# Performance work log

Hardware: AMD Instinct MI355X
Metric: run time of the kernel (lower is better)

Reference implementation:

```python
import jax, jax.numpy as jnp
import numpy as np

N = 50000      # nodes
E = 800000     # edges (avg degree 16)
F_IN = 256
F_OUT = 256


def setup_inputs() -> dict:
    key = jax.random.key(0)
    ks = jax.random.split(key, 8)
    feature = jax.random.normal(ks[0], (N, F_IN), dtype=jnp.float32)
    e_w = jax.random.uniform(ks[1], (E, 1), dtype=jnp.float32)
    snorm_n = jnp.ones((N, 1), dtype=jnp.float32)
    snorm_e = jnp.ones((E, 1), dtype=jnp.float32)
    src = jax.random.randint(ks[2], (E,), 0, N, dtype=jnp.int32)
    dst = jax.random.randint(ks[3], (E,), 0, N, dtype=jnp.int32)
    scale = 1.0 / np.sqrt(F_IN)
    W_self = jax.random.normal(ks[4], (F_IN, F_OUT), dtype=jnp.float32) * scale
    W = jax.random.normal(ks[5], (F_IN, F_OUT), dtype=jnp.float32) * scale
    b = jax.random.normal(ks[6], (F_OUT,), dtype=jnp.float32) * scale
    return {"feature": feature, "e_w": e_w, "snorm_n": snorm_n,
            "snorm_e": snorm_e, "W_self": W_self, "W": W, "b": b,
            "src": src, "dst": dst}


def reference(feature, e_w, snorm_n, snorm_e, W_self, W, b, src, dst):
    n = feature.shape[0]
    ones_e = jnp.ones_like(src, dtype=feature.dtype)
    # self transform
    h_s = feature @ W_self                                   # [N, F_OUT]
    # source-side degree normalization: deg_out^{-1/2}
    out_deg = jnp.maximum(jax.ops.segment_sum(ones_e, src, num_segments=n), 1.0)
    feat = feature * (out_deg ** -0.5)[:, None]              # [N, F_IN]
    # message = h[src] * e_w, aggregated by sum into dst (u_mul_e + sum reduce)
    msgs = feat[src] * e_w                                   # [E, F_IN]
    agg = jax.ops.segment_sum(msgs, dst, num_segments=n)     # [N, F_IN]
    # neighbor transform + destination-side degree normalization
    h = agg @ W + b                                          # [N, F_OUT]
    in_deg = jnp.maximum(jax.ops.segment_sum(ones_e, dst, num_segments=n), 1.0)
    h = h * (in_deg ** -0.5)[:, None]
    return h_s + h, e_w
```

## Files before the change

kernel.cpp:

```cpp
#include <hip/hip_runtime.h>
#include <hip/hip_bf16.h>

#define N_NODES 50000
#define N_EDGES 800000

#define ROW_TILES    391
#define K1_BLOCKS    2352
#define WCONV_BLOCKS 512
#define SCAN_BLOCKS  196
#define EDGE_BLOCKS  782

typedef __bf16 bf16x8_t __attribute__((ext_vector_type(8)));
typedef float  f32x4_t  __attribute__((ext_vector_type(4)));
typedef unsigned short u16x8 __attribute__((ext_vector_type(8)));
typedef unsigned int   u32x4 __attribute__((ext_vector_type(4)));

__device__ __forceinline__ unsigned short f2bf(float x) {
  __hip_bfloat16 h = __float2bfloat16(x);
  return __builtin_bit_cast(unsigned short, h);
}
__device__ __forceinline__ float bf2f(unsigned short u) {
  unsigned int v = ((unsigned int)u) << 16;
  return __builtin_bit_cast(float, v);
}
__device__ __forceinline__ unsigned int pk2(float lo, float hi) {
  return ((unsigned int)f2bf(hi) << 16) | (unsigned int)f2bf(lo);
}
__device__ __forceinline__ bf16x8_t cvt8(float4 lo, float4 hi) {
  u32x4 u;
  u.x = pk2(lo.x, lo.y); u.y = pk2(lo.z, lo.w);
  u.z = pk2(hi.x, hi.y); u.w = pk2(hi.z, hi.w);
  return __builtin_bit_cast(bf16x8_t, u);
}

__global__ __launch_bounds__(256) void wconv_kernel(
    const float* __restrict__ Wself, const float* __restrict__ W,
    unsigned short* __restrict__ Bt)
{
  int idx = blockIdx.x * 256 + threadIdx.x;
  int n = idx >> 8, k = idx & 255;
  float v = (n < 256) ? Wself[k * 256 + n] : W[k * 256 + (n - 256)];
  Bt[idx] = f2bf(v);
}

__global__ __launch_bounds__(256, 4) void gemm_edge_kernel(
    const float* __restrict__ feature,
    const unsigned short* __restrict__ Bt,
    const float* __restrict__ e_w, const int* __restrict__ src, const int* __restrict__ dst,
    int* __restrict__ cnt_in, int* __restrict__ cnt_out,
    unsigned char* __restrict__ rank8, float* __restrict__ out1,
    unsigned short* __restrict__ hs16,
    unsigned char* __restrict__ y8)
{
  const int b   = blockIdx.x;
  const int tid = threadIdx.x;
  const int w   = b / 48;
  const int o   = (b % 48) >> 3;
  const int r   = b & 7;

  if (o == 2 || o == 5) {
    const int h = w * 16 + r + ((o == 5) ? 8 : 0);
    if (h >= EDGE_BLOCKS) return;
    const int e0 = h * 1024 + tid;
#pragma unroll
    for (int k = 0; k < 4; ++k) {
      int e = e0 + k * 256;
      if (e < N_EDGES) {
        int s = src[e], d = dst[e];
        out1[e] = e_w[e];
        atomicAdd(&cnt_out[s], 1);
        rank8[e] = (unsigned char)atomicAdd(&cnt_in[d], 1);
      }
    }
    return;
  }

  const int q = o - (o > 2 ? 1 : 0);
  const int t = w * 8 + r;
  if (t >= ROW_TILES) return;

  const int m0   = t * 128;
  const int bn0  = q * 128;
  const int lane = tid & 63;
  const int wave = tid >> 6;
  const int wm   = (wave & 1) * 64;
  const int wn   = (wave >> 1) * 64;
  const int fr   = lane & 15;
  const int fkc  = lane >> 4;

  const float* ap[4];
  const unsigned short* bp[4];
#pragma unroll
  for (int i = 0; i < 4; ++i) {
    int row = m0 + wm + i * 16 + fr;
    row = (row < N_NODES) ? row : 0;
    ap[i] = feature + (size_t)row * 256 + fkc * 8;
  }
#pragma unroll
  for (int j = 0; j < 4; ++j)
    bp[j] = Bt + (size_t)(bn0 + wn + j * 16 + fr) * 256 + fkc * 8;

  f32x4_t acc[4][4] = {};

  for (int s = 0; s < 8; ++s) {
    const int k0 = s * 32;
    bf16x8_t av[4], bv[4];
#pragma unroll
    for (int i = 0; i < 4; ++i) {
      float4 lo = *(const float4*)(ap[i] + k0);
      float4 hi = *(const float4*)(ap[i] + k0 + 4);
      av[i] = cvt8(lo, hi);
    }
#pragma unroll
    for (int j = 0; j < 4; ++j)
      bv[j] = *(const bf16x8_t*)(bp[j] + k0);
#pragma unroll
    for (int i = 0; i < 4; ++i)
#pragma unroll
      for (int j = 0; j < 4; ++j)
        acc[i][j] = __builtin_amdgcn_mfma_f32_16x16x32_bf16(av[i], bv[j], acc[i][j], 0, 0, 0);
  }

  if (q < 2) {
    const int cbase = q * 128 + wn + (lane & 15);
#pragma unroll
    for (int i = 0; i < 4; ++i) {
      int rowb = m0 + wm + i * 16 + (lane >> 4) * 4;
#pragma unroll
      for (int j = 0; j < 4; ++j) {
        int col = cbase + j * 16;
#pragma unroll
        for (int rr = 0; rr < 4; ++rr) {
          int row = rowb + rr;
          if (row < N_NODES)
            hs16[(size_t)row * 256 + col] = f2bf(acc[i][j][rr]);
        }
      }
    }
  } else {
    const int cbase = (q - 2) * 128 + wn + (lane & 15);
#pragma unroll
    for (int i = 0; i < 4; ++i) {
      int rowb = m0 + wm + i * 16 + (lane >> 4) * 4;
#pragma unroll
      for (int j = 0; j < 4; ++j) {
        int col = cbase + j * 16;
#pragma unroll
        for (int rr = 0; rr < 4; ++rr) {
          int row = rowb + rr;
          if (row < N_NODES) {
            float ys = acc[i][j][rr];
            unsigned int pk = (unsigned int)__builtin_amdgcn_cvt_pk_fp8_f32(ys, ys, 0, false);
            y8[(size_t)row * 256 + col] = (unsigned char)(pk & 0xffu);
          }
        }
      }
    }
  }
}

__global__ __launch_bounds__(256) void scan1_kernel(
    const int* __restrict__ cnt, int* __restrict__ sums)
{
  int idx = blockIdx.x * 256 + threadIdx.x;
  int v = (idx < N_NODES) ? cnt[idx] : 0;
#pragma unroll
  for (int d = 32; d; d >>= 1) v += __shfl_down(v, d);
  __shared__ int sm[4];
  if ((threadIdx.x & 63) == 0) sm[threadIdx.x >> 6] = v;
  __syncthreads();
  if (threadIdx.x == 0) sums[blockIdx.x] = sm[0] + sm[1] + sm[2] + sm[3];
}

__global__ __launch_bounds__(256) void scan2_kernel(int* __restrict__ sums)
{
  const int t = threadIdx.x;
  int v = (t < SCAN_BLOCKS) ? sums[t] : 0;
  __shared__ int sm[256];
  sm[t] = v;
  __syncthreads();
  for (int d = 1; d < 256; d <<= 1) {
    int u = (t >= d) ? sm[t - d] : 0;
    __syncthreads();
    sm[t] += u;
    __syncthreads();
  }
  if (t < SCAN_BLOCKS) sums[t] = sm[t] - v;
}

__global__ __launch_bounds__(256) void scan3_kernel(
    const int* __restrict__ cnt, const int* __restrict__ sums, int* __restrict__ off)
{
  const int t = threadIdx.x;
  int idx = blockIdx.x * 256 + t;
  int v = (idx < N_NODES) ? cnt[idx] : 0;
  __shared__ int sm[256];
  sm[t] = v;
  __syncthreads();
  for (int d = 1; d < 256; d <<= 1) {
    int u = (t >= d) ? sm[t - d] : 0;
    __syncthreads();
    sm[t] += u;
    __syncthreads();
  }
  if (idx <= N_NODES) off[idx] = sm[t] - v + sums[blockIdx.x];
}

__global__ __launch_bounds__(256) void scatter_kernel(
    const float* __restrict__ e_w, const int* __restrict__ src, const int* __restrict__ dst,
    const unsigned char* __restrict__ rank8, const int* __restrict__ off,
    unsigned int* __restrict__ csr)
{
  const int e0 = blockIdx.x * 1024 + threadIdx.x;
#pragma unroll
  for (int k = 0; k < 4; ++k) {
    int e = e0 + k * 256;
    if (e < N_EDGES) {
      int d = dst[e];
      int r = rank8[e];
      float w = e_w[e];
      int s = src[e];
      csr[off[d] + r] = ((unsigned int)f2bf(w) << 16) | (unsigned int)s;
    }
  }
}

__global__ __launch_bounds__(256) void agg_kernel(
    const unsigned char* __restrict__ y8, const unsigned int* __restrict__ csr,
    const int* __restrict__ off, const int* __restrict__ cnt_out,
    const unsigned short* __restrict__ hs16,
    const float* __restrict__ bias, float* __restrict__ out0)
{
  const int hw   = threadIdx.x >> 5;
  const int lane = threadIdx.x & 31;
  const int node = blockIdx.x * 8 + hw;
  if (node >= N_NODES) return;
  const int base = off[node];
  const int deg  = off[node + 1] - base;

  float a0 = 0.f, a1 = 0.f, a2 = 0.f, a3 = 0.f;
  float a4 = 0.f, a5 = 0.f, a6 = 0.f, a7 = 0.f;

  for (int bb = 0; bb < deg; bb += 32) {
    int idx = bb + lane;
    unsigned int ent = (idx < deg) ? csr[base + idx] : 0u;
    int   sl = (int)(ent & 0xffffu);
    float wl = bf2f((unsigned short)(ent >> 16));
    int co = cnt_out[sl]; if (co < 1) co = 1;
    wl *= rsqrtf((float)co);

#pragma unroll
    for (int t0 = 0; t0 < 32; t0 += 16) {
      if (bb + t0 >= deg) break;
#pragma unroll
      for (int t = 0; t < 16; ++t) {
        int eb = t0 + t;
        int   s = __shfl(sl, eb, 32);
        float w = __shfl(wl, eb, 32);
        uint2 u = *(const uint2*)(y8 + (size_t)s * 256 + lane * 8);
        a0 += w * __builtin_amdgcn_cvt_f32_fp8(u.x, 0);
        a1 += w * __builtin_amdgcn_cvt_f32_fp8(u.x, 1);
        a2 += w * __builtin_amdgcn_cvt_f32_fp8(u.x, 2);
        a3 += w * __builtin_amdgcn_cvt_f32_fp8(u.x, 3);
        a4 += w * __builtin_amdgcn_cvt_f32_fp8(u.y, 0);
        a5 += w * __builtin_amdgcn_cvt_f32_fp8(u.y, 1);
        a6 += w * __builtin_amdgcn_cvt_f32_fp8(u.y, 2);
        a7 += w * __builtin_amdgcn_cvt_f32_fp8(u.y, 3);
      }
    }
  }

  int dn = deg < 1 ? 1 : deg;
  float inv = rsqrtf((float)dn);
  size_t offo = (size_t)node * 256 + lane * 8;
  u16x8 hv = *(const u16x8*)(hs16 + offo);
  float4 b0 = *(const float4*)(bias + lane * 8);
  float4 b1 = *(const float4*)(bias + lane * 8 + 4);
  float4 o0, o1;
  o0.x = bf2f(hv[0]) + (a0 + b0.x) * inv;
  o0.y = bf2f(hv[1]) + (a1 + b0.y) * inv;
  o0.z = bf2f(hv[2]) + (a2 + b0.z) * inv;
  o0.w = bf2f(hv[3]) + (a3 + b0.w) * inv;
  o1.x = bf2f(hv[4]) + (a4 + b1.x) * inv;
  o1.y = bf2f(hv[5]) + (a5 + b1.y) * inv;
  o1.z = bf2f(hv[6]) + (a6 + b1.z) * inv;
  o1.w = bf2f(hv[7]) + (a7 + b1.w) * inv;
  *(float4*)(out0 + offo)     = o0;
  *(float4*)(out0 + offo + 4) = o1;
}

extern "C" void kernel_launch(void* const* d_in, const int* in_sizes, int n_in,
                              void* d_out, int out_size, void* d_ws, size_t ws_size,
                              hipStream_t stream) {
  const float* feature = (const float*)d_in[0];
  const float* e_w     = (const float*)d_in[1];
  const float* W_self  = (const float*)d_in[4];
  const float* W       = (const float*)d_in[5];
  const float* bias    = (const float*)d_in[6];
  const int*   src     = (const int*)d_in[7];
  const int*   dst     = (const int*)d_in[8];

  float* out0 = (float*)d_out;
  float* out1 = out0 + (size_t)N_NODES * 256;

  char* ws = (char*)d_ws;
  int*            cnt_in  = (int*)(ws + 0);
  int*            cnt_out = (int*)(ws + 262144);
  int*            off     = (int*)(ws + 524288);
  unsigned char*  rank8   = (unsigned char*)(ws + 786432);
  int*            sums    = (int*)(ws + 1638400);
  unsigned int*   csr     = (unsigned int*)(ws + 1835008);
  unsigned short* Bt      = (unsigned short*)(ws + 5242880);
  unsigned char*  y8      = (unsigned char*)(ws + 5767168);
  unsigned short* hs16    = (unsigned short*)(ws + 18567168);

  hipMemsetAsync(ws, 0, 524288, stream);

  wconv_kernel<<<WCONV_BLOCKS, 256, 0, stream>>>(W_self, W, Bt);
  gemm_edge_kernel<<<K1_BLOCKS, 256, 0, stream>>>(
      feature, Bt, e_w, src, dst, cnt_in, cnt_out, rank8, out1, hs16, y8);
  scan1_kernel<<<SCAN_BLOCKS, 256, 0, stream>>>(cnt_in, sums);
  scan2_kernel<<<1, 256, 0, stream>>>(sums);
  scan3_kernel<<<SCAN_BLOCKS, 256, 0, stream>>>(cnt_in, sums, off);
  scatter_kernel<<<EDGE_BLOCKS, 256, 0, stream>>>(e_w, src, dst, rank8, off, csr);
  agg_kernel<<<(N_NODES + 7) / 8, 256, 0, stream>>>(y8, csr, off, cnt_out, hs16, bias, out0);
}
```

Baseline: 304.8 us.

## Stage B tile in swizzled LDS, preload A, fold out-degree norm into CSR

Result: faster. 290.0 us (-4.9%).

```diff
diff --git a/kernel.cpp b/kernel.cpp
--- a/kernel.cpp
+++ b/kernel.cpp
@@ -43,7 +43,7 @@
   Bt[idx] = f2bf(v);
 }
 
-__global__ __launch_bounds__(256, 4) void gemm_edge_kernel(
+__global__ __launch_bounds__(256, 2) void gemm_edge_kernel(
     const float* __restrict__ feature,
     const unsigned short* __restrict__ Bt,
     const float* __restrict__ e_w, const int* __restrict__ src, const int* __restrict__ dst,
@@ -75,6 +75,8 @@
     return;
   }
 
+  __shared__ __align__(16) unsigned short Bs[128 * 256];
+
   const int q = o - (o > 2 ? 1 : 0);
   const int t = w * 8 + r;
   if (t >= ROW_TILES) return;
@@ -88,37 +90,51 @@
   const int fr   = lane & 15;
   const int fkc  = lane >> 4;
 
+#pragma unroll
+  for (int m = 0; m < 16; ++m) {
+    int L  = m * 256 + tid;
+    int rr = L >> 5, cs = L & 31;
+    int cg = cs ^ (rr & 7);
+    const unsigned short* gb = Bt + (size_t)(bn0 + rr) * 256 + cg * 8;
+    __builtin_amdgcn_global_load_lds((const __attribute__((address_space(1))) void*)gb,
+                                     (__attribute__((address_space(3))) void*)&Bs[(size_t)L * 8],
+                                     16, 0, 0);
+  }
+
   const float* ap[4];
-  const unsigned short* bp[4];
 #pragma unroll
   for (int i = 0; i < 4; ++i) {
     int row = m0 + wm + i * 16 + fr;
     row = (row < N_NODES) ? row : 0;
     ap[i] = feature + (size_t)row * 256 + fkc * 8;
   }
-#pragma unroll
-  for (int j = 0; j < 4; ++j)
-    bp[j] = Bt + (size_t)(bn0 + wn + j * 16 + fr) * 256 + fkc * 8;
+  bf16x8_t Areg[8][4];
+#pragma unroll
+  for (int s = 0; s < 8; ++s)
+#pragma unroll
+    for (int i = 0; i < 4; ++i) {
+      float4 lo = *(const float4*)(ap[i] + s * 32);
+      float4 hi = *(const float4*)(ap[i] + s * 32 + 4);
+      Areg[s][i] = cvt8(lo, hi);
+    }
+
+  __syncthreads();
 
   f32x4_t acc[4][4] = {};
-
+#pragma unroll
   for (int s = 0; s < 8; ++s) {
-    const int k0 = s * 32;
-    bf16x8_t av[4], bv[4];
-#pragma unroll
-    for (int i = 0; i < 4; ++i) {
-      float4 lo = *(const float4*)(ap[i] + k0);
-      float4 hi = *(const float4*)(ap[i] + k0 + 4);
-      av[i] = cvt8(lo, hi);
-    }
-#pragma unroll
-    for (int j = 0; j < 4; ++j)
-      bv[j] = *(const bf16x8_t*)(bp[j] + k0);
+    bf16x8_t bv[4];
+#pragma unroll
+    for (int j = 0; j < 4; ++j) {
+      int R  = wn + j * 16 + fr;
+      int cs = (s * 4 + fkc) ^ (R & 7);
+      bv[j] = *(const bf16x8_t*)&Bs[R * 256 + cs * 8];
+    }
 #pragma unroll
     for (int i = 0; i < 4; ++i)
 #pragma unroll
       for (int j = 0; j < 4; ++j)
-        acc[i][j] = __builtin_amdgcn_mfma_f32_16x16x32_bf16(av[i], bv[j], acc[i][j], 0, 0, 0);
+        acc[i][j] = __builtin_amdgcn_mfma_f32_16x16x32_bf16(Areg[s][i], bv[j], acc[i][j], 0, 0, 0);
   }
 
   if (q < 2) {
@@ -209,7 +225,7 @@
 __global__ __launch_bounds__(256) void scatter_kernel(
     const float* __restrict__ e_w, const int* __restrict__ src, const int* __restrict__ dst,
     const unsigned char* __restrict__ rank8, const int* __restrict__ off,
-    unsigned int* __restrict__ csr)
+    const int* __restrict__ cnt_out, unsigned int* __restrict__ csr)
 {
   const int e0 = blockIdx.x * 1024 + threadIdx.x;
 #pragma unroll
@@ -218,8 +234,9 @@
     if (e < N_EDGES) {
       int d = dst[e];
       int r = rank8[e];
-      float w = e_w[e];
       int s = src[e];
+      int co = cnt_out[s]; if (co < 1) co = 1;
+      float w = e_w[e] * rsqrtf((float)co);
       csr[off[d] + r] = ((unsigned int)f2bf(w) << 16) | (unsigned int)s;
     }
   }
@@ -227,8 +244,7 @@
 
 __global__ __launch_bounds__(256) void agg_kernel(
     const unsigned char* __restrict__ y8, const unsigned int* __restrict__ csr,
-    const int* __restrict__ off, const int* __restrict__ cnt_out,
-    const unsigned short* __restrict__ hs16,
+    const int* __restrict__ off, const unsigned short* __restrict__ hs16,
     const float* __restrict__ bias, float* __restrict__ out0)
 {
   const int hw   = threadIdx.x >> 5;
@@ -246,14 +262,12 @@
     unsigned int ent = (idx < deg) ? csr[base + idx] : 0u;
     int   sl = (int)(ent & 0xffffu);
     float wl = bf2f((unsigned short)(ent >> 16));
-    int co = cnt_out[sl]; if (co < 1) co = 1;
-    wl *= rsqrtf((float)co);
-
-#pragma unroll
-    for (int t0 = 0; t0 < 32; t0 += 16) {
+
+#pragma unroll
+    for (int t0 = 0; t0 < 32; t0 += 8) {
       if (bb + t0 >= deg) break;
 #pragma unroll
-      for (int t = 0; t < 16; ++t) {
+      for (int t = 0; t < 8; ++t) {
         int eb = t0 + t;
         int   s = __shfl(sl, eb, 32);
         float w = __shfl(wl, eb, 32);
@@ -322,6 +336,6 @@
   scan1_kernel<<<SCAN_BLOCKS, 256, 0, stream>>>(cnt_in, sums);
   scan2_kernel<<<1, 256, 0, stream>>>(sums);
   scan3_kernel<<<SCAN_BLOCKS, 256, 0, stream>>>(cnt_in, sums, off);
-  scatter_kernel<<<EDGE_BLOCKS, 256, 0, stream>>>(e_w, src, dst, rank8, off, csr);
-  agg_kernel<<<(N_NODES + 7) / 8, 256, 0, stream>>>(y8, csr, off, cnt_out, hs16, bias, out0);
-}
+  scatter_kernel<<<EDGE_BLOCKS, 256, 0, stream>>>(e_w, src, dst, rank8, off, cnt_out, csr);
+  agg_kernel<<<(N_NODES + 7) / 8, 256, 0, stream>>>(y8, csr, off, hs16, bias, out0);
+}
```
